# Optimization experiments

Hardware: AMD Instinct MI355X
Metric: run time of the kernel (lower is better)

## Reference

```python
import jax, jax.numpy as jnp
import numpy as np

ANNEAL = 0.01
N, D, NUM_CLASSES = 384, 128, 24


def setup_inputs() -> dict:
    key = jax.random.key(0)
    k1, k2 = jax.random.split(key)
    preds = jax.random.normal(k1, (N, D), dtype=jnp.float32)
    # L2-normalize embeddings (standard for SmoothAP cosine similarities)
    preds = preds / jnp.linalg.norm(preds, axis=1, keepdims=True)
    labels = jax.random.randint(k2, (N,), 0, NUM_CLASSES, dtype=jnp.int64)
    return {"preds": preds, "labels": labels}


def reference(preds, labels):
    n = preds.shape[0]
    dt = preds.dtype
    eye = jnp.eye(n, dtype=dt)
    # I_pos[i,j] = 1 iff same label and i != j (lmu.get_all_pairs_indices)
    I_pos = (labels[:, None] == labels[None, :]).astype(dt) * (1 - eye)
    sim = preds @ preds.T                              # [N, N]
    # sim_diff[a,b,c] = sim[a,c] - sim[a,b]  (unsqueeze(1) - unsqueeze(2))
    diff = sim[:, None, :] - sim[:, :, None]           # [N, N, N]
    sg = jax.nn.sigmoid(jnp.clip(diff / ANNEAL, -50.0, 50.0))
    sg = sg * (1 - eye)                                # zero where b == c
    # sum_c sg[a,b,c] * I_pos[a,c], then gate by I_pos[a,b]
    pos_sum = jnp.einsum('abc,ac->ab', sg, I_pos) * I_pos
    sim_pos_rk = 1 + I_pos + pos_sum                   # [N, N]
    sim_all_rk = 1 + jnp.sum(sg, axis=-1)              # [N, N]
    n_pos = jnp.sum(I_pos, axis=1) + 1                 # [N]
    per_i = jnp.sum(sim_pos_rk / sim_all_rk, axis=1) / n_pos
    ap = jnp.sum(jnp.where(n_pos > 1, per_i, jnp.zeros((), dt))) / n
    return (1 - ap)[None]                              # shape (1,), like torch
```

## Files before the change

### kernel.cpp

```cpp
#include <hip/hip_runtime.h>

#define N 384
#define NT 768
#define HJ 48

__device__ const float KLOG2E = 144.26950408889634f;
__device__ const float CL = 63.0f;

__global__ __launch_bounds__(NT) void smoothap_fused(const float* __restrict__ preds,
                                                     const int* __restrict__ labels,
                                                     float* __restrict__ out) {
    __shared__ __align__(16) float4 s_pa[32];
    __shared__ __align__(16) float2 s_AP[N];
    __shared__ __align__(16) float  s_E[N];
    __shared__ __align__(16) float2 s_part[N];
    __shared__ int   s_wpos[12];
    __shared__ float s_red[12];
    __shared__ int   s_P;

    const int a = blockIdx.x;
    const int t = threadIdx.x;
    const int lane = t & 63;
    const int wid = t >> 6;

    if (t < 32) s_pa[t] = ((const float4*)(preds + (size_t)a * 128))[t];
    __syncthreads();

    const int c = t >> 1;
    const int h = t & 1;
    float posf_t = 0.f, E_t = 0.f;
    {
        const float4* pt = (const float4*)(preds + (size_t)c * 128) + h * 16;
        const float4* wa = s_pa + h * 16;
        float acc0 = 0.f, acc1 = 0.f;
#pragma unroll
        for (int k = 0; k < 16; k += 2) {
            float4 v0 = pt[k],     w0 = wa[k];
            float4 v1 = pt[k + 1], w1 = wa[k + 1];
            acc0 = fmaf(v0.x, w0.x, acc0); acc0 = fmaf(v0.y, w0.y, acc0);
            acc0 = fmaf(v0.z, w0.z, acc0); acc0 = fmaf(v0.w, w0.w, acc0);
            acc1 = fmaf(v1.x, w1.x, acc1); acc1 = fmaf(v1.y, w1.y, acc1);
            acc1 = fmaf(v1.z, w1.z, acc1); acc1 = fmaf(v1.w, w1.w, acc1);
        }
        float acc = acc0 + acc1;
        acc += __shfl_xor(acc, 1);
        posf_t = (labels[c] == labels[a] && c != a) ? 1.f : 0.f;
        const float x = fminf(fmaxf(acc * KLOG2E, -CL), CL);
        if (h == 0) {
            const float A_t = __builtin_amdgcn_exp2f(x);
            s_AP[c] = make_float2(A_t, posf_t);
        } else {
            E_t = __builtin_amdgcn_exp2f(-x);
        }
        unsigned long long m = __ballot(h == 1 && posf_t > 0.5f);
        if (lane == 0) s_wpos[wid] = __popcll(m);
    }
    __syncthreads();

    {
        int base = 0, P = 0;
#pragma unroll
        for (int w = 0; w < 12; ++w) {
            int cnt = s_wpos[w];
            if (w < wid) base += cnt;
            P += cnt;
        }
        if (h == 1) {
            unsigned long long m = __ballot(posf_t > 0.5f);
            const int mlt = __popcll(m & ((1ull << lane) - 1ull));
            const int cin = lane >> 1;
            const int dest = (posf_t > 0.5f) ? (base + mlt)
                                             : (P + wid * 32 - base + cin - mlt);
            s_E[dest] = E_t;
        }
        if (t == 0) s_P = P;
    }
    __syncthreads();

    const int chalf = (t >= N) ? 1 : 0;
    const int b = t - chalf * N;
    const float2 ap = s_AP[b];
    const float A = ap.x;
    const float posf = ap.y;
    const int Ps = __builtin_amdgcn_readfirstlane(s_P);

    float all_sum = 0.f, pos_sum = 0.f;
    const float4* sE4 = (const float4*)s_E;
    const int jlo = chalf * HJ, jhi = jlo + HJ;
    const int jPfull = Ps >> 2;
    const int rem = Ps & 3;

    int j = jlo;
    const int e1 = (jhi < jPfull) ? jhi : jPfull;
#pragma unroll 4
    for (; j < e1; ++j) {
        float4 q = sE4[j];
        float s0 = __builtin_amdgcn_rcpf(fmaf(A, q.x, 1.f));
        float s1 = __builtin_amdgcn_rcpf(fmaf(A, q.y, 1.f));
        float s2 = __builtin_amdgcn_rcpf(fmaf(A, q.z, 1.f));
        float s3 = __builtin_amdgcn_rcpf(fmaf(A, q.w, 1.f));
        const float s = (s0 + s1) + (s2 + s3);
        all_sum += s;
        pos_sum += s;
    }
    if (j == jPfull && j < jhi && rem) {
        float4 q = sE4[j];
        const float qv[4] = {q.x, q.y, q.z, q.w};
#pragma unroll
        for (int k = 0; k < 4; ++k) {
            float sg = __builtin_amdgcn_rcpf(fmaf(A, qv[k], 1.f));
            all_sum += sg;
            if (k < rem) pos_sum += sg;
        }
        ++j;
    }
#pragma unroll 4
    for (; j < jhi; ++j) {
        float4 q = sE4[j];
        float s0 = __builtin_amdgcn_rcpf(fmaf(A, q.x, 1.f));
        float s1 = __builtin_amdgcn_rcpf(fmaf(A, q.y, 1.f));
        float s2 = __builtin_amdgcn_rcpf(fmaf(A, q.z, 1.f));
        float s3 = __builtin_amdgcn_rcpf(fmaf(A, q.w, 1.f));
        all_sum += (s0 + s1) + (s2 + s3);
    }

    if (chalf) s_part[b] = make_float2(all_sum, pos_sum);
    __syncthreads();

    float r = 0.f;
    if (t < N) {
        const float2 o = s_part[b];
        const float all = all_sum + o.x - 0.5f;
        const float pos = pos_sum + o.y - 0.5f * posf;
        r = fmaf(posf, 1.f + pos, 1.f) * __builtin_amdgcn_rcpf(1.f + all);
    }

    float rr = r;
#pragma unroll
    for (int off = 32; off; off >>= 1) rr += __shfl_down(rr, off);
    if (lane == 0) s_red[wid] = rr;
    __syncthreads();
    if (t == 0) {
        float rs = 0.f;
#pragma unroll
        for (int w = 0; w < 12; ++w) rs += s_red[w];
        const int P = s_P;
        float contrib = (P > 0) ? (-rs / ((float)(P + 1) * (float)N)) : 0.f;
        if (a == 0) contrib += 1.f;
        atomicAdd(out, contrib);
    }
}

extern "C" void kernel_launch(void* const* d_in, const int* in_sizes, int n_in,
                              void* d_out, int out_size, void* d_ws, size_t ws_size,
                              hipStream_t stream) {
    const float* preds = (const float*)d_in[0];
    const int* labels = (const int*)d_in[1];
    float* out = (float*)d_out;

    smoothap_fused<<<N, NT, 0, stream>>>(preds, labels, out);
}
```

Baseline: 71.99 us.

## Register-block four b rows per thread and reduce c-slices with shuffles

Each thread now handles four b rows against a 12-float4 slice of the sorted E vector. Eight lanes split the c range and combine their partial sums with xor shuffles, replacing the two-half split that merged through shared memory. Each LDS load of E is reused across four rows, which cuts LDS traffic per sigmoid and removes a barrier and the s_part buffer. The cost is more registers per thread and the shuffle reduction overhead.

```diff
diff --git a/kernel.cpp b/kernel.cpp
--- a/kernel.cpp
+++ b/kernel.cpp
@@ -2,7 +2,6 @@
 
 #define N 384
 #define NT 768
-#define HJ 48
 
 __device__ const float KLOG2E = 144.26950408889634f;
 __device__ const float CL = 63.0f;
@@ -13,7 +12,6 @@
     __shared__ __align__(16) float4 s_pa[32];
     __shared__ __align__(16) float2 s_AP[N];
     __shared__ __align__(16) float  s_E[N];
-    __shared__ __align__(16) float2 s_part[N];
     __shared__ int   s_wpos[12];
     __shared__ float s_red[12];
     __shared__ int   s_P;
@@ -77,16 +75,19 @@
     }
     __syncthreads();
 
-    const int chalf = (t >= N) ? 1 : 0;
-    const int b = t - chalf * N;
-    const float2 ap = s_AP[b];
-    const float A = ap.x;
-    const float posf = ap.y;
+    const int bq = t >> 3;
+    const int cs = t & 7;
+    const float4* sAP4 = (const float4*)s_AP;
+    const float4 ap01 = sAP4[bq * 2];
+    const float4 ap23 = sAP4[bq * 2 + 1];
+    const float A0 = ap01.x, p0 = ap01.y, A1 = ap01.z, p1 = ap01.w;
+    const float A2 = ap23.x, p2 = ap23.y, A3 = ap23.z, p3 = ap23.w;
     const int Ps = __builtin_amdgcn_readfirstlane(s_P);
 
-    float all_sum = 0.f, pos_sum = 0.f;
+    float all0 = 0.f, all1 = 0.f, all2 = 0.f, all3 = 0.f;
+    float pos0 = 0.f, pos1 = 0.f, pos2 = 0.f, pos3 = 0.f;
     const float4* sE4 = (const float4*)s_E;
-    const int jlo = chalf * HJ, jhi = jlo + HJ;
+    const int jlo = cs * 12, jhi = jlo + 12;
     const int jPfull = Ps >> 2;
     const int rem = Ps & 3;
 
@@ -94,45 +95,66 @@
     const int e1 = (jhi < jPfull) ? jhi : jPfull;
 #pragma unroll 4
     for (; j < e1; ++j) {
-        float4 q = sE4[j];
-        float s0 = __builtin_amdgcn_rcpf(fmaf(A, q.x, 1.f));
-        float s1 = __builtin_amdgcn_rcpf(fmaf(A, q.y, 1.f));
-        float s2 = __builtin_amdgcn_rcpf(fmaf(A, q.z, 1.f));
-        float s3 = __builtin_amdgcn_rcpf(fmaf(A, q.w, 1.f));
-        const float s = (s0 + s1) + (s2 + s3);
-        all_sum += s;
-        pos_sum += s;
-    }
-    if (j == jPfull && j < jhi && rem) {
-        float4 q = sE4[j];
+        const float4 q = sE4[j];
         const float qv[4] = {q.x, q.y, q.z, q.w};
 #pragma unroll
         for (int k = 0; k < 4; ++k) {
-            float sg = __builtin_amdgcn_rcpf(fmaf(A, qv[k], 1.f));
-            all_sum += sg;
-            if (k < rem) pos_sum += sg;
+            const float e = qv[k];
+            const float s0 = __builtin_amdgcn_rcpf(fmaf(A0, e, 1.f));
+            const float s1 = __builtin_amdgcn_rcpf(fmaf(A1, e, 1.f));
+            const float s2 = __builtin_amdgcn_rcpf(fmaf(A2, e, 1.f));
+            const float s3 = __builtin_amdgcn_rcpf(fmaf(A3, e, 1.f));
+            all0 += s0; all1 += s1; all2 += s2; all3 += s3;
+            pos0 += s0; pos1 += s1; pos2 += s2; pos3 += s3;
+        }
+    }
+    if (j == jPfull && j < jhi && rem) {
+        const float4 q = sE4[j];
+        const float qv[4] = {q.x, q.y, q.z, q.w};
+#pragma unroll
+        for (int k = 0; k < 4; ++k) {
+            const float e = qv[k];
+            const float s0 = __builtin_amdgcn_rcpf(fmaf(A0, e, 1.f));
+            const float s1 = __builtin_amdgcn_rcpf(fmaf(A1, e, 1.f));
+            const float s2 = __builtin_amdgcn_rcpf(fmaf(A2, e, 1.f));
+            const float s3 = __builtin_amdgcn_rcpf(fmaf(A3, e, 1.f));
+            all0 += s0; all1 += s1; all2 += s2; all3 += s3;
+            if (k < rem) { pos0 += s0; pos1 += s1; pos2 += s2; pos3 += s3; }
         }
         ++j;
     }
 #pragma unroll 4
     for (; j < jhi; ++j) {
-        float4 q = sE4[j];
-        float s0 = __builtin_amdgcn_rcpf(fmaf(A, q.x, 1.f));
-        float s1 = __builtin_amdgcn_rcpf(fmaf(A, q.y, 1.f));
-        float s2 = __builtin_amdgcn_rcpf(fmaf(A, q.z, 1.f));
-        float s3 = __builtin_amdgcn_rcpf(fmaf(A, q.w, 1.f));
-        all_sum += (s0 + s1) + (s2 + s3);
+        const float4 q = sE4[j];
+        const float qv[4] = {q.x, q.y, q.z, q.w};
+#pragma unroll
+        for (int k = 0; k < 4; ++k) {
+            const float e = qv[k];
+            all0 += __builtin_amdgcn_rcpf(fmaf(A0, e, 1.f));
+            all1 += __builtin_amdgcn_rcpf(fmaf(A1, e, 1.f));
+            all2 += __builtin_amdgcn_rcpf(fmaf(A2, e, 1.f));
+            all3 += __builtin_amdgcn_rcpf(fmaf(A3, e, 1.f));
+        }
     }
 
-    if (chalf) s_part[b] = make_float2(all_sum, pos_sum);
-    __syncthreads();
+#pragma unroll
+    for (int m = 1; m <= 4; m <<= 1) {
+        all0 += __shfl_xor(all0, m); pos0 += __shfl_xor(pos0, m);
+        all1 += __shfl_xor(all1, m); pos1 += __shfl_xor(pos1, m);
+        all2 += __shfl_xor(all2, m); pos2 += __shfl_xor(pos2, m);
+        all3 += __shfl_xor(all3, m); pos3 += __shfl_xor(pos3, m);
+    }
 
     float r = 0.f;
-    if (t < N) {
-        const float2 o = s_part[b];
-        const float all = all_sum + o.x - 0.5f;
-        const float pos = pos_sum + o.y - 0.5f * posf;
-        r = fmaf(posf, 1.f + pos, 1.f) * __builtin_amdgcn_rcpf(1.f + all);
+    if (cs == 0) {
+        const float a0 = all0 - 0.5f, q0 = pos0 - 0.5f * p0;
+        const float a1 = all1 - 0.5f, q1 = pos1 - 0.5f * p1;
+        const float a2 = all2 - 0.5f, q2 = pos2 - 0.5f * p2;
+        const float a3 = all3 - 0.5f, q3 = pos3 - 0.5f * p3;
+        r  = fmaf(p0, 1.f + q0, 1.f) * __builtin_amdgcn_rcpf(1.f + a0);
+        r += fmaf(p1, 1.f + q1, 1.f) * __builtin_amdgcn_rcpf(1.f + a1);
+        r += fmaf(p2, 1.f + q2, 1.f) * __builtin_amdgcn_rcpf(1.f + a2);
+        r += fmaf(p3, 1.f + q3, 1.f) * __builtin_amdgcn_rcpf(1.f + a3);
     }
 
     float rr = r;
```

New measurement: 75.86 us. 1.05x slower.
